# Kernel optimization log

Hardware: AMD Instinct MI355X
Metric: run time of the kernel (lower is better)

The kernel has to match this reference:

```python
import jax, jax.numpy as jnp
import numpy as np

H = 512
IN_CH = 3
DIM = 32
FILTER_SIZES = [4, 4, 2]
OUT_DIM = 1
BATCH = 128


def _patchify(x, f):
    # (B, C, D, D) -> (B, C, P, P, f*f) non-overlapping patches (matches torch unfold+reshape)
    B, C, D, _ = x.shape
    P = D // f
    xp = x.reshape(B, C, P, f, P, f).transpose(0, 1, 2, 4, 3, 5)
    return xp.reshape(B, C, P, P, f * f)


def _loc_block(x, w, f):
    # w: (O, C, P, P, f*f) -- per-patch unshared filters
    C = x.shape[1]
    xp = _patchify(x, f)
    y = jnp.einsum('bcpqf,ocpqf->bopq', xp, w)
    return jax.nn.relu(y / (f * f * C) ** 0.5)


def setup_inputs() -> dict:
    key = jax.random.key(0)
    ks = jax.random.split(key, 5)
    f1, f2, f3 = FILTER_SIZES
    P1 = DIM // f1            # 8
    P2 = P1 // f2             # 2
    P3 = P2 // f3             # 1
    x = jax.random.normal(ks[0], (BATCH, IN_CH, DIM, DIM), dtype=jnp.float32)
    w1 = jax.random.normal(ks[1], (H, IN_CH, P1, P1, f1 * f1), dtype=jnp.float32)
    w2 = jax.random.normal(ks[2], (H, H, P2, P2, f2 * f2), dtype=jnp.float32)
    w3 = jax.random.normal(ks[3], (H, H, P3, P3, f3 * f3), dtype=jnp.float32)
    beta = jax.random.normal(ks[4], (H * P3 * P3, OUT_DIM), dtype=jnp.float32)
    return {'x': x, 'w1': w1, 'w2': w2, 'w3': w3, 'beta': beta}


def reference(x, w1, w2, w3, beta):
    f1, f2, f3 = FILTER_SIZES
    y = _loc_block(x, w1, f1)
    y = _loc_block(y, w2, f2)
    y = _loc_block(y, w3, f3)
    y = y.reshape(y.shape[0], -1)
    return y @ beta / beta.shape[0] ** 0.5
```

## Files before the change

kernel.cpp:

```cpp
#include <hip/hip_runtime.h>


typedef _Float16 f16;
typedef _Float16 half8 __attribute__((ext_vector_type(8)));
typedef _Float16 half4 __attribute__((ext_vector_type(4)));
typedef float f32x4 __attribute__((ext_vector_type(4)));

#define SWZ(r, c) ((((r) << 6) + (c)) ^ (((r) & 7) << 3))
#define SWZL(r, c) ((((r) << 10) + (c)) ^ (((r) & 7) << 3))

#define GLOAD_LDS16(G, L)                                                     \
  __builtin_amdgcn_global_load_lds(                                           \
      (const __attribute__((address_space(1))) void*)(G),                     \
      (__attribute__((address_space(3))) void*)(L), 16, 0, 0)

__global__ __launch_bounds__(256) void l1_mfma(const float* __restrict__ x,
                                               const float* __restrict__ w1,
                                               f16* __restrict__ A2) {
  const int o0 = blockIdx.x << 5;
  const int s2 = blockIdx.y;
  const int b0 = blockIdx.z << 5;
  const int p2 = s2 >> 1, q2 = s2 & 1;
  __shared__ __align__(16) f16 Xs[32 * 1024];
  __shared__ __align__(16) f16 Ws[32 * 1024];
  const int t = threadIdx.x;

#pragma unroll
  for (int i = 0; i < 8; ++i) {
    int e = (i << 8) + t;
    int row = e >> 6, rem = e & 63, g = rem >> 2, j = rem & 3;
    half4 z = {};
    *(half4*)&Xs[SWZL(row, g * 64 + 48 + j * 4)] = z;
    *(half4*)&Ws[SWZL(row, g * 64 + 48 + j * 4)] = z;
  }
#pragma unroll
  for (int i = 0; i < 24; ++i) {
    int fl = (i << 8) + t;
    int b = fl / 192, rem = fl % 192;
    int c = rem >> 6, rem2 = rem & 63;
    int a = rem2 >> 4, fi = (rem2 >> 2) & 3, bq = rem2 & 3;
    float4 v = *(const float4*)(x + ((size_t)(b0 + b) * 3 + c) * 1024 +
                                (p2 * 16 + a * 4 + fi) * 32 + q2 * 16 + bq * 4);
    half4 h;
    h[0] = (f16)v.x; h[1] = (f16)v.y; h[2] = (f16)v.z; h[3] = (f16)v.w;
    *(half4*)&Xs[SWZL(b, (a * 4 + bq) * 64 + c * 16 + fi * 4)] = h;
  }
#pragma unroll
  for (int i = 0; i < 24; ++i) {
    int fl = (i << 8) + t;
    int o = fl / 192, rem = fl % 192;
    int c = rem >> 6, rem2 = rem & 63;
    int g = rem2 >> 2, f4 = rem2 & 3;
    float4 v = *(const float4*)(w1 + (size_t)(o0 + o) * 3072 + c * 1024 +
                                (p2 * 4 + (g >> 2)) * 128 + (q2 * 4 + (g & 3)) * 16 + f4 * 4);
    half4 h;
    h[0] = (f16)v.x; h[1] = (f16)v.y; h[2] = (f16)v.z; h[3] = (f16)v.w;
    *(half4*)&Ws[SWZL(o, g * 64 + c * 16 + f4 * 4)] = h;
  }
  __syncthreads();

  const int wv = t >> 6, ln = t & 63;
  const int bw = wv >> 1, ow = wv & 1;
  const int frow = ln & 15, fr4 = ln >> 4;
  f32x4 acc[16] = {};
#pragma unroll
  for (int g = 0; g < 16; ++g) {
#pragma unroll
    for (int ks = 0; ks < 2; ++ks) {
      half8 a = *(const half8*)&Xs[SWZL(bw * 16 + frow, g * 64 + ks * 32 + fr4 * 8)];
      half8 b = *(const half8*)&Ws[SWZL(ow * 16 + frow, g * 64 + ks * 32 + fr4 * 8)];
      acc[g] = __builtin_amdgcn_mfma_f32_16x16x32_f16(a, b, acc[g], 0, 0, 0);
    }
  }
  f16* A2b = A2 + (size_t)s2 * 128 * 8192;
#pragma unroll
  for (int r = 0; r < 4; ++r) {
    int b = b0 + bw * 16 + fr4 * 4 + r;
    int o = o0 + ow * 16 + frow;
    f16 tmp[16];
#pragma unroll
    for (int g = 0; g < 16; ++g)
      tmp[g] = (f16)fmaxf(acc[g][r] * 0.14433756729740643f, 0.f);
    f16* dst = A2b + (size_t)b * 8192 + o * 16;
    *(half8*)dst = *(half8*)&tmp[0];
    *(half8*)(dst + 8) = *(half8*)&tmp[8];
  }
}

template <int MODE>
__global__ __launch_bounds__(256) void gemm_f16(const f16* __restrict__ A,
                                                const float* __restrict__ W,
                                                float* __restrict__ P) {
  __shared__ __align__(16) f16 As[2][128 * 64];
  __shared__ __align__(16) float Bs[2][64 * 64];
  const int t = threadIdx.x;
  const int bid = blockIdx.x;
  constexpr int AK = (MODE == 0) ? 8192 : 2048;
  constexpr int ITERS = (MODE == 0) ? 8 : 2;
  const int s = (MODE == 0) ? (bid >> 7) : 0;
  const int kc = (MODE == 0) ? ((bid >> 3) & 15) : (bid >> 3);
  const int n = bid & 7;
  const int kb0 = kc * (ITERS * 64);
  const f16* Ab = A + (size_t)(MODE == 0 ? s * 128 : 0) * AK + kb0;
  const int o0 = n << 6;

  const int wv = t >> 6, ln = t & 63;
  const int a_r = (ln >> 3), a_sg0 = ln & 7;
  const int b_r = (ln >> 4), b_sg0 = ln & 15;

#define STAGE(IT, BUF)                                                          \
  {                                                                             \
    _Pragma("unroll") for (int jj = 0; jj < 4; ++jj) {                          \
      int rbase = wv * 32 + jj * 8;                                             \
      int r = rbase + a_r;                                                      \
      int sg = a_sg0 ^ (r & 7);                                                 \
      GLOAD_LDS16(Ab + (size_t)r * AK + ((IT) << 6) + (sg << 3),                \
                  &As[BUF][rbase << 6]);                                        \
    }                                                                           \
    _Pragma("unroll") for (int jj = 0; jj < 4; ++jj) {                          \
      int rbase = wv * 16 + jj * 4;                                             \
      int r = rbase + b_r;                                                      \
      int sg = b_sg0 ^ (r & 7);                                                 \
      const float* gp;                                                          \
      if constexpr (MODE == 0) {                                                \
        int k = kb0 + ((IT) << 6) + (sg << 2);                                  \
        gp = W + (size_t)(o0 + r) * 32768 + ((k >> 4) << 6) + (s << 4) + (k & 15); \
      } else {                                                                  \
        gp = W + (size_t)(o0 + r) * 2048 + kb0 + ((IT) << 6) + (sg << 2);       \
      }                                                                         \
      GLOAD_LDS16(gp, &Bs[BUF][rbase << 6]);                                    \
    }                                                                           \
  }

  const int wr = wv >> 1, wc = wv & 1;
  const int frow = ln & 15, fr4 = ln >> 4;
  f32x4 acc[4][2] = {};

#define COMPUTE(BUF)                                                            \
  _Pragma("unroll") for (int ks = 0; ks < 2; ++ks) {                            \
    half8 a[4];                                                                 \
    _Pragma("unroll") for (int mi = 0; mi < 4; ++mi) {                          \
      int r = wr * 64 + mi * 16 + frow;                                         \
      int gl = ((ks << 2) + fr4) ^ (r & 7);                                     \
      a[mi] = *(const half8*)&As[BUF][(r << 6) + (gl << 3)];                    \
    }                                                                           \
    _Pragma("unroll") for (int ni = 0; ni < 2; ++ni) {                          \
      int r = wc * 32 + ni * 16 + frow;                                         \
      int s0 = (ks << 3) + (fr4 << 1);                                          \
      float4 f0 = *(const float4*)&Bs[BUF][(r << 6) + ((s0 ^ (r & 7)) << 2)];   \
      float4 f1 = *(const float4*)&Bs[BUF][(r << 6) + (((s0 + 1) ^ (r & 7)) << 2)]; \
      half8 hb;                                                                 \
      hb[0] = (f16)f0.x; hb[1] = (f16)f0.y; hb[2] = (f16)f0.z; hb[3] = (f16)f0.w; \
      hb[4] = (f16)f1.x; hb[5] = (f16)f1.y; hb[6] = (f16)f1.z; hb[7] = (f16)f1.w; \
      _Pragma("unroll") for (int mi = 0; mi < 4; ++mi)                          \
        acc[mi][ni] = __builtin_amdgcn_mfma_f32_16x16x32_f16(a[mi], hb, acc[mi][ni], 0, 0, 0); \
    }                                                                           \
  }

  STAGE(0, 0)
#pragma unroll
  for (int it = 0; it < ITERS; ++it) {
    const int cur = it & 1;
    if (it + 1 < ITERS) {
      STAGE(it + 1, cur ^ 1)
      asm volatile("s_waitcnt vmcnt(8)" ::: "memory");
    } else {
      asm volatile("s_waitcnt vmcnt(0)" ::: "memory");
    }
    __builtin_amdgcn_s_barrier();
    __builtin_amdgcn_sched_barrier(0);
    COMPUTE(cur)
    __builtin_amdgcn_sched_barrier(0);
    __builtin_amdgcn_s_barrier();
  }

  float* Pb = P + (size_t)(MODE == 0 ? (kc << 2) + s : kc) * 65536;
#pragma unroll
  for (int mi = 0; mi < 4; ++mi)
#pragma unroll
    for (int ni = 0; ni < 2; ++ni)
#pragma unroll
      for (int r = 0; r < 4; ++r) {
        int gm = wr * 64 + mi * 16 + fr4 * 4 + r;
        int gn = o0 + wc * 32 + ni * 16 + frow;
        Pb[(size_t)gm * 512 + gn] = acc[mi][ni][r];
      }
#undef STAGE
#undef COMPUTE
}

__global__ __launch_bounds__(256) void reduce2(const float* __restrict__ P2,
                                               f16* __restrict__ A3) {
  int idx = blockIdx.x * 256 + threadIdx.x;
  int og = idx & 127, b = idx >> 7;
  f16 outv[16];
#pragma unroll
  for (int s = 0; s < 4; ++s) {
    float4 acc = {0.f, 0.f, 0.f, 0.f};
#pragma unroll
    for (int kc = 0; kc < 16; ++kc) {
      float4 v = *(const float4*)(P2 + (size_t)((kc << 2) + s) * 65536 + b * 512 + og * 4);
      acc.x += v.x; acc.y += v.y; acc.z += v.z; acc.w += v.w;
    }
    outv[0 * 4 + s] = (f16)fmaxf(acc.x * 0.011048543456039805f, 0.f);
    outv[1 * 4 + s] = (f16)fmaxf(acc.y * 0.011048543456039805f, 0.f);
    outv[2 * 4 + s] = (f16)fmaxf(acc.z * 0.011048543456039805f, 0.f);
    outv[3 * 4 + s] = (f16)fmaxf(acc.w * 0.011048543456039805f, 0.f);
  }
  f16* dst = A3 + (size_t)b * 2048 + og * 16;
  *(half8*)dst = *(half8*)&outv[0];
  *(half8*)(dst + 8) = *(half8*)&outv[8];
}

__global__ __launch_bounds__(256) void out_fused(const float* __restrict__ P3,
                                                 const float* __restrict__ beta,
                                                 float* __restrict__ out) {
  const int b = blockIdx.x, t = threadIdx.x;
  float acc = 0.f;
#pragma unroll
  for (int oi = 0; oi < 2; ++oi) {
    int o = (oi << 8) + t;
    float v = 0.f;
#pragma unroll
    for (int kc = 0; kc < 16; ++kc) v += P3[(size_t)kc * 65536 + b * 512 + o];
    acc += fmaxf(v * 0.022097086912079608f, 0.f) * beta[o];
  }
  __shared__ float red[4];
#pragma unroll
  for (int off = 32; off > 0; off >>= 1) acc += __shfl_down(acc, off);
  if ((t & 63) == 0) red[t >> 6] = acc;
  __syncthreads();
  if (t == 0) out[b] = (red[0] + red[1] + red[2] + red[3]) * 0.044194173824159216f;
}

extern "C" void kernel_launch(void* const* d_in, const int* in_sizes, int n_in,
                              void* d_out, int out_size, void* d_ws, size_t ws_size,
                              hipStream_t stream) {
  const float* x    = (const float*)d_in[0];
  const float* w1   = (const float*)d_in[1];
  const float* w2   = (const float*)d_in[2];
  const float* w3   = (const float*)d_in[3];
  const float* beta = (const float*)d_in[4];
  float* out = (float*)d_out;

  char* wsb = (char*)d_ws;
  f16*   A2 = (f16*)wsb;
  float* P2 = (float*)(wsb + (8ull << 20));
  f16*   A3 = (f16*)(wsb + (24ull << 20));
  float* P3 = (float*)(wsb + (24ull << 20) + (1ull << 19));

  l1_mfma<<<dim3(16, 4, 4), 256, 0, stream>>>(x, w1, A2);
  gemm_f16<0><<<512, 256, 0, stream>>>(A2, w2, P2);
  reduce2<<<64, 256, 0, stream>>>(P2, A3);
  gemm_f16<1><<<128, 256, 0, stream>>>(A3, w3, P3);
  out_fused<<<128, 256, 0, stream>>>(P3, beta, out);
}
```

Baseline: 49.44 us.

## Fuse layer-2 split-K reduction into GEMM via last-block atomic counter

Removes the separate reduce2 launch. Each gemm_f16<0> block now increments a per-column-tile counter after writing its partials, and the last of the 64 blocks for that tile sums P2 and writes the ReLU'd fp16 A3 slice. The counters are reset by the first block of l1_mfma. This saves one kernel launch and its gap, at the cost of serialising the reduction onto 8 tail blocks, which may lengthen the GEMM tail.

```diff
diff --git a/kernel.cpp b/kernel.cpp
--- a/kernel.cpp
+++ b/kernel.cpp
@@ -16,15 +16,17 @@
 
 __global__ __launch_bounds__(256) void l1_mfma(const float* __restrict__ x,
                                                const float* __restrict__ w1,
-                                               f16* __restrict__ A2) {
+                                               f16* __restrict__ A2,
+                                               int* __restrict__ ctr) {
+  const int t = threadIdx.x;
+  if (blockIdx.x == 0 && blockIdx.y == 0 && blockIdx.z == 0 && t < 8)
+    ctr[t] = 0;
   const int o0 = blockIdx.x << 5;
   const int s2 = blockIdx.y;
   const int b0 = blockIdx.z << 5;
   const int p2 = s2 >> 1, q2 = s2 & 1;
   __shared__ __align__(16) f16 Xs[32 * 1024];
   __shared__ __align__(16) f16 Ws[32 * 1024];
-  const int t = threadIdx.x;
-
 #pragma unroll
   for (int i = 0; i < 8; ++i) {
     int e = (i << 8) + t;
@@ -87,12 +89,36 @@
   }
 }
 
+__device__ __forceinline__ void reduce2_cell(int b, int og, const float* __restrict__ P2,
+                                             f16* __restrict__ A3) {
+  f16 outv[16];
+#pragma unroll
+  for (int s = 0; s < 4; ++s) {
+    float4 a4 = {0.f, 0.f, 0.f, 0.f};
+#pragma unroll
+    for (int kc = 0; kc < 16; ++kc) {
+      float4 v = *(const float4*)(P2 + (size_t)((kc << 2) + s) * 65536 + b * 512 + og * 4);
+      a4.x += v.x; a4.y += v.y; a4.z += v.z; a4.w += v.w;
+    }
+    outv[0 * 4 + s] = (f16)fmaxf(a4.x * 0.011048543456039805f, 0.f);
+    outv[1 * 4 + s] = (f16)fmaxf(a4.y * 0.011048543456039805f, 0.f);
+    outv[2 * 4 + s] = (f16)fmaxf(a4.z * 0.011048543456039805f, 0.f);
+    outv[3 * 4 + s] = (f16)fmaxf(a4.w * 0.011048543456039805f, 0.f);
+  }
+  f16* dst = A3 + (size_t)b * 2048 + og * 16;
+  *(half8*)dst = *(half8*)&outv[0];
+  *(half8*)(dst + 8) = *(half8*)&outv[8];
+}
+
 template <int MODE>
 __global__ __launch_bounds__(256) void gemm_f16(const f16* __restrict__ A,
                                                 const float* __restrict__ W,
-                                                float* __restrict__ P) {
+                                                float* __restrict__ P,
+                                                f16* __restrict__ A3,
+                                                int* __restrict__ ctr) {
   __shared__ __align__(16) f16 As[2][128 * 64];
   __shared__ __align__(16) float Bs[2][64 * 64];
+  __shared__ int lastf;
   const int t = threadIdx.x;
   const int bid = blockIdx.x;
   constexpr int AK = (MODE == 0) ? 8192 : 2048;
@@ -103,7 +129,6 @@
   const int kb0 = kc * (ITERS * 64);
   const f16* Ab = A + (size_t)(MODE == 0 ? s * 128 : 0) * AK + kb0;
   const int o0 = n << 6;
-
   const int wv = t >> 6, ln = t & 63;
   const int a_r = (ln >> 3), a_sg0 = ln & 7;
   const int b_r = (ln >> 4), b_sg0 = ln & 15;
@@ -185,49 +210,45 @@
         int gn = o0 + wc * 32 + ni * 16 + frow;
         Pb[(size_t)gm * 512 + gn] = acc[mi][ni][r];
       }
+
+  if constexpr (MODE == 0) {
+    __threadfence();
+    if (t == 0) lastf = (atomicAdd(&ctr[n], 1) == 63) ? 1 : 0;
+    __syncthreads();
+    if (lastf) {
+      __threadfence();
+      for (int idx = t; idx < 2048; idx += 256) {
+        int ogl = idx & 15, b = idx >> 4;
+        reduce2_cell(b, (n << 4) + ogl, P, A3);
+      }
+    }
+  }
 #undef STAGE
 #undef COMPUTE
 }
 
-__global__ __launch_bounds__(256) void reduce2(const float* __restrict__ P2,
-                                               f16* __restrict__ A3) {
-  int idx = blockIdx.x * 256 + threadIdx.x;
-  int og = idx & 127, b = idx >> 7;
-  f16 outv[16];
-#pragma unroll
-  for (int s = 0; s < 4; ++s) {
-    float4 acc = {0.f, 0.f, 0.f, 0.f};
-#pragma unroll
-    for (int kc = 0; kc < 16; ++kc) {
-      float4 v = *(const float4*)(P2 + (size_t)((kc << 2) + s) * 65536 + b * 512 + og * 4);
-      acc.x += v.x; acc.y += v.y; acc.z += v.z; acc.w += v.w;
-    }
-    outv[0 * 4 + s] = (f16)fmaxf(acc.x * 0.011048543456039805f, 0.f);
-    outv[1 * 4 + s] = (f16)fmaxf(acc.y * 0.011048543456039805f, 0.f);
-    outv[2 * 4 + s] = (f16)fmaxf(acc.z * 0.011048543456039805f, 0.f);
-    outv[3 * 4 + s] = (f16)fmaxf(acc.w * 0.011048543456039805f, 0.f);
-  }
-  f16* dst = A3 + (size_t)b * 2048 + og * 16;
-  *(half8*)dst = *(half8*)&outv[0];
-  *(half8*)(dst + 8) = *(half8*)&outv[8];
+__device__ __forceinline__ float head_partial(int b, int t, const float* __restrict__ P3,
+                                              const float* __restrict__ beta) {
+  float acc = 0.f;
+#pragma unroll
+  for (int oi = 0; oi < 2; ++oi) {
+    int o = (oi << 8) + t;
+    float v = 0.f;
+#pragma unroll
+    for (int kc = 0; kc < 16; ++kc) v += P3[(size_t)kc * 65536 + b * 512 + o];
+    acc += fmaxf(v * 0.022097086912079608f, 0.f) * beta[o];
+  }
+#pragma unroll
+  for (int off = 32; off > 0; off >>= 1) acc += __shfl_down(acc, off);
+  return acc;
 }
 
 __global__ __launch_bounds__(256) void out_fused(const float* __restrict__ P3,
                                                  const float* __restrict__ beta,
                                                  float* __restrict__ out) {
+  __shared__ float red[4];
   const int b = blockIdx.x, t = threadIdx.x;
-  float acc = 0.f;
-#pragma unroll
-  for (int oi = 0; oi < 2; ++oi) {
-    int o = (oi << 8) + t;
-    float v = 0.f;
-#pragma unroll
-    for (int kc = 0; kc < 16; ++kc) v += P3[(size_t)kc * 65536 + b * 512 + o];
-    acc += fmaxf(v * 0.022097086912079608f, 0.f) * beta[o];
-  }
-  __shared__ float red[4];
-#pragma unroll
-  for (int off = 32; off > 0; off >>= 1) acc += __shfl_down(acc, off);
+  float acc = head_partial(b, t, P3, beta);
   if ((t & 63) == 0) red[t >> 6] = acc;
   __syncthreads();
   if (t == 0) out[b] = (red[0] + red[1] + red[2] + red[3]) * 0.044194173824159216f;
@@ -248,10 +269,10 @@
   float* P2 = (float*)(wsb + (8ull << 20));
   f16*   A3 = (f16*)(wsb + (24ull << 20));
   float* P3 = (float*)(wsb + (24ull << 20) + (1ull << 19));
-
-  l1_mfma<<<dim3(16, 4, 4), 256, 0, stream>>>(x, w1, A2);
-  gemm_f16<0><<<512, 256, 0, stream>>>(A2, w2, P2);
-  reduce2<<<64, 256, 0, stream>>>(P2, A3);
-  gemm_f16<1><<<128, 256, 0, stream>>>(A3, w3, P3);
+  int*  ctr = (int*)(wsb + (28ull << 20) + (1ull << 19));
+
+  l1_mfma<<<dim3(16, 4, 4), 256, 0, stream>>>(x, w1, A2, ctr);
+  gemm_f16<0><<<512, 256, 0, stream>>>(A2, w2, P2, A3, ctr);
+  gemm_f16<1><<<128, 256, 0, stream>>>(A3, w3, P3, nullptr, nullptr);
   out_fused<<<128, 256, 0, stream>>>(P3, beta, out);
 }
```

Measured after the change: 127.0 us. 157% more time.
